# Optimization experiments

Measured on AMD Instinct MI355X. Metric: run time of the kernel, lower is better.

## Reference

```python
import jax, jax.numpy as jnp
import numpy as np

D, H, K, L, NB = 128, 8, 16, 16, 2
N, E, MN, ME = 100_000, 800_000, 1_000, 8_000
VOCAB, BT, VP = 50_000, 256, 15
_SQD, _SQK = float(np.sqrt(D)), float(np.sqrt(K))


def _segment_softmax(score, seg, num):
    m = jax.ops.segment_max(score, seg, num_segments=num)
    e = jnp.exp(score - m[seg])
    z = jax.ops.segment_sum(e, seg, num_segments=num)
    return e / (z[seg] + 1e-9)


def _meta_learner(feat, u, W2, W1):
    # latent-attention factorization: feat [n,D] -> 2d param [n,H,K], 1d param [n,H]
    w = jax.nn.softmax((feat @ u.T) / _SQD, axis=-1)  # [n,L]
    return jnp.einsum('nl,lhk->nhk', w, W2), w @ W1


def _conv(feat, src, dst, p2n, p1n, p2e, p1e, Wq, Wk, Wv, Wo):
    # HeteroAttnConv: multi-head attention message passing modulated by
    # per-node (p2n,p1n) and per-edge (p2e,p1e) meta parameters.
    n = feat.shape[0]
    q = (feat @ Wq).reshape(n, H, K) * p2n
    kf = (feat @ Wk).reshape(n, H, K)
    v = (feat @ Wv).reshape(n, H, K)
    ke = kf[src] * p2e                                   # [e,H,K]
    score = (q[dst] * ke).sum(-1) / _SQK + p1e + p1n[dst]  # [e,H]
    attn = _segment_softmax(score, dst, n)
    agg = jax.ops.segment_sum(attn[..., None] * v[src], dst, num_segments=n).reshape(n, D)
    return jax.nn.relu(agg @ Wo), ke.reshape(-1, D)


def _forward(emb, u, W2lat, W1lat, Wq_m, Wk_m, Wv_m, Wo_m, Wq, Wk, Wv, Wo,
             node_vals, meta_node_vals, src, dst, meta_src, meta_dst,
             meta_node_id, meta_edge_id, target_idx,
             static_vals, static_src, static_dst):
    # _init_meta_param: static param-name graph, copy_u/sum then meta_learner
    fs = emb[static_vals]
    agg = jax.ops.segment_sum(fs[static_src], static_dst, num_segments=VP)
    p2s, p1s = _meta_learner(agg, u, W2lat, W1lat)
    base_tw, base_n1, base_n2 = p1s[0], p1s[3], p2s[6]   # target_weight, node 1d, node 2d
    base_e1, base_e2 = p1s[9], p2s[12]                   # edge 1d, edge 2d

    meta_feat = emb[meta_node_vals]
    feat = emb[node_vals]
    # _asign_param_to_graph(meta_graph): broadcast base buffers only
    mp2n = jnp.broadcast_to(base_n2, (MN, H, K))
    mp1n = jnp.broadcast_to(base_n1, (MN, H))
    mp2e = jnp.broadcast_to(base_e2, (ME, H, K))
    mp1e = jnp.broadcast_to(base_e1, (ME, H))

    out = jnp.zeros((BT, 1), feat.dtype)
    for b in range(NB):
        pre_meta, pre = meta_feat, feat
        meta_feat, meta_edge_feat = _conv(meta_feat, meta_src, meta_dst,
                                          mp2n, mp1n, mp2e, mp1e,
                                          Wq_m[b], Wk_m[b], Wv_m[b], Wo_m[b])
        # _asign_param_to_graph(graph, meta_node_feat, meta_edge_feat):
        # base repeat + indexed add of meta_learner outputs
        p2mn, p1mn = _meta_learner(meta_feat, u, W2lat, W1lat)
        p2me, p1me = _meta_learner(meta_edge_feat, u, W2lat, W1lat)
        p2n = base_n2[None] + p2mn[meta_node_id]
        p1n = base_n1[None] + p1mn[meta_node_id]
        tw = base_tw[None] + p1mn[meta_node_id]
        p2e = base_e2[None] + p2me[meta_edge_id]
        p1e = base_e1[None] + p1me[meta_edge_id]
        feat, _ = _conv(feat, src, dst, p2n, p1n, p2e, p1e,
                        Wq[b], Wk[b], Wv[b], Wo[b])
        # block residual
        meta_feat = meta_feat + pre_meta
        feat = feat + pre
        # Target: per-target-node weighted readout with target_weight param
        logit = jnp.einsum('th,thk->t', tw[target_idx],
                           feat[target_idx].reshape(BT, H, K))
        out = out + logit[:, None]
    return out / NB


def setup_inputs() -> dict:
    key = jax.random.key(0)
    ks = jax.random.split(key, 24)
    s = 0.05
    inp = {}
    inp['emb'] = jax.random.normal(ks[0], (VOCAB, D), jnp.float32) * s
    inp['u'] = jax.random.normal(ks[1], (L, D), jnp.float32) * s
    inp['W2lat'] = jax.random.normal(ks[2], (L, H, K), jnp.float32) * s
    inp['W1lat'] = jax.random.normal(ks[3], (L, H), jnp.float32) * s
    for i, nm in enumerate(['Wq_m', 'Wk_m', 'Wv_m', 'Wo_m', 'Wq', 'Wk', 'Wv', 'Wo']):
        inp[nm] = jax.random.normal(ks[4 + i], (NB, D, D), jnp.float32) / np.sqrt(D)
    inp['node_vals'] = jax.random.randint(ks[12], (N,), 0, VOCAB)
    inp['meta_node_vals'] = jax.random.randint(ks[13], (MN,), 0, VOCAB)
    inp['src'] = jax.random.randint(ks[14], (E,), 0, N)
    inp['dst'] = jax.random.randint(ks[15], (E,), 0, N)
    inp['meta_src'] = jax.random.randint(ks[16], (ME,), 0, MN)
    inp['meta_dst'] = jax.random.randint(ks[17], (ME,), 0, MN)
    inp['meta_node_id'] = jax.random.randint(ks[18], (N,), 0, MN)
    inp['meta_edge_id'] = jax.random.randint(ks[19], (E,), 0, ME)
    inp['target_idx'] = jax.random.randint(ks[20], (BT,), 0, N)
    # static param-name graph: 5 names x (1 name node + 2 token nodes), tokens->name
    name_pos = np.arange(5) * 3
    inp['static_vals'] = jax.random.randint(ks[21], (VP,), 0, VOCAB)
    inp['static_src'] = jnp.asarray(np.stack([name_pos + 1, name_pos + 2], 1).reshape(-1), jnp.int32)
    inp['static_dst'] = jnp.asarray(np.repeat(name_pos, 2), jnp.int32)
    return inp


def reference(emb, u, W2lat, W1lat, Wq_m, Wk_m, Wv_m, Wo_m, Wq, Wk, Wv, Wo,
              node_vals, meta_node_vals, src, dst, meta_src, meta_dst,
              meta_node_id, meta_edge_id, target_idx,
              static_vals, static_src, static_dst):
    return _forward(emb, u, W2lat, W1lat, Wq_m, Wk_m, Wv_m, Wo_m, Wq, Wk, Wv, Wo,
                    node_vals, meta_node_vals, src, dst, meta_src, meta_dst,
                    meta_node_id, meta_edge_id, target_idx,
                    static_vals, static_src, static_dst)
```

## Files before the change

### kernel.cpp

```cpp
#include <hip/hip_runtime.h>
#include <hip/hip_bf16.h>
#include <hip/hip_fp8.h>

#define DD   128
#define HH   8

typedef short bf16x8 __attribute__((ext_vector_type(8)));
typedef float f32x4  __attribute__((ext_vector_type(4)));
typedef float f32x2  __attribute__((ext_vector_type(2)));

__device__ __forceinline__ float b2f(unsigned short v){
  union { unsigned int u; float f; } x; x.u = ((unsigned int)v) << 16; return x.f;
}
__device__ __forceinline__ unsigned short f2b(float f){
  __hip_bfloat16 h = __float2bfloat16(f);
  return *(unsigned short*)&h;
}
__device__ __forceinline__ unsigned char f2f8(float x){
  __hip_fp8_e4m3 h(x);
  return h.__x;
}
__device__ __forceinline__ float f82f(unsigned char b){
  __hip_fp8_e4m3 h; h.__x = b;
  return (float)h;
}
__device__ __forceinline__ void cvt4(unsigned int w, float* o){
#if defined(__has_builtin)
# if __has_builtin(__builtin_amdgcn_cvt_pk_f32_fp8)
  f32x2 lo = __builtin_amdgcn_cvt_pk_f32_fp8((int)w, false);
  f32x2 hi = __builtin_amdgcn_cvt_pk_f32_fp8((int)w, true);
  o[0]=lo[0]; o[1]=lo[1]; o[2]=hi[0]; o[3]=hi[1];
  return;
# endif
#endif
  o[0]=f82f(w&0xff); o[1]=f82f((w>>8)&0xff);
  o[2]=f82f((w>>16)&0xff); o[3]=f82f((w>>24)&0xff);
}
struct __align__(8) us4 { unsigned short x,y,z,w; };
struct __align__(16) us8 { unsigned short s[8]; };

__device__ __forceinline__ float gld(const void* p, size_t i, bool f32){
  if (f32) return ((const float*)p)[i];
  return b2f(((const unsigned short*)p)[i]);
}

__device__ __forceinline__ void gll16(const void* g, void* l){
  __builtin_amdgcn_global_load_lds(
      (const __attribute__((address_space(1))) unsigned int*)g,
      (__attribute__((address_space(3))) unsigned int*)l, 16, 0, 0);
}

struct WPtrs { const void* p[8]; };

enum { EPI_STORE=0, EPI_SCALE_CONST=1, EPI_RELU=3,
       EPI_RELU_RES=4, EPI_RELU_RES2=5 };

#define CPAD 132

template<int EPI, bool INB, bool OUTB>
__global__ __launch_bounds__(256) void gemm128m(
    const void* __restrict__ Av, const unsigned short* __restrict__ Bt,
    void* __restrict__ Cv, int M,
    const unsigned short* __restrict__ Rb,
    const float* __restrict__ Rf, float* __restrict__ C2,
    const int* __restrict__ mnid, const float* __restrict__ p1mn,
    const float* __restrict__ base,
    const int* __restrict__ tgt_of, const int* __restrict__ tgt_next,
    float* __restrict__ acc)
{
  __shared__ __align__(16) unsigned short Asb[64*128];
  __shared__ __align__(16) unsigned short Btb[16896];
  const int tid = threadIdx.x;
  const int wave = tid >> 6, lane = tid & 63;
  const int row0 = blockIdx.x * 64;

  if (INB){
    const char* Ab = (const char*)Av;
    int n4 = lane >> 4, c = lane & 15;
#pragma unroll
    for (int op=0; op<4; op++){
      int rA = wave*16 + op*4;
      int n = rA + n4;
      int gr = row0 + n; if (gr >= M) gr = M - 1;
      gll16(Ab + (size_t)gr*256 + ((size_t)((c ^ (n & 7)) << 4)), &Asb[rA*128]);
    }
  } else {
    const float* Af = (const float*)Av;
    int r = tid >> 2, cb = (tid & 3) * 32, rx = (r & 7) << 3;
    int gr = row0 + r;
#pragma unroll
    for (int j=0;j<8;j++){
      int cc = cb + j*4;
      float4 val = make_float4(0.f,0.f,0.f,0.f);
      if (gr < M) val = *(const float4*)(Af + (size_t)gr*DD + cc);
      us4 o; o.x=f2b(val.x); o.y=f2b(val.y); o.z=f2b(val.z); o.w=f2b(val.w);
      *(us4*)&Asb[r*128 + (cc ^ rx)] = o;
    }
  }
  {
    int n4 = lane >> 4, c = lane & 15;
#pragma unroll
    for (int op=0; op<8; op++){
      int rB = wave*32 + op*4;
      int n = rB + n4;
      gll16((const char*)Bt + (size_t)n*256 + ((size_t)((c ^ (n & 7)) << 4)),
            &Btb[rB*128]);
    }
  }
  __syncthreads();

  f32x4 acc0[8];
#pragma unroll
  for (int t=0;t<8;t++) acc0[t] = (f32x4){0.f,0.f,0.f,0.f};
  const int am = (lane & 15), kq = (lane >> 4) * 8, axr = (am & 7) << 3;
#pragma unroll
  for (int k0=0;k0<128;k0+=32){
    int xo = (k0 + kq) ^ axr;
    bf16x8 a = *(bf16x8*)&Asb[(wave*16 + am)*128 + xo];
#pragma unroll
    for (int t=0;t<8;t++){
      bf16x8 b = *(bf16x8*)&Btb[(t*16 + am)*128 + xo];
      acc0[t] = __builtin_amdgcn_mfma_f32_16x16x32_bf16(a, b, acc0[t], 0,0,0);
    }
  }
  __syncthreads();
  float* Cls = (float*)Btb;
  {
    int rr = wave*16 + (lane>>4)*4;
    int cc = lane & 15;
#pragma unroll
    for (int t=0;t<8;t++)
#pragma unroll
      for (int r=0;r<4;r++)
        Cls[(rr + r)*CPAD + t*16 + cc] = acc0[t][r];
  }
  __syncthreads();

  {
    int r = tid >> 2, cb = (tid & 3) * 32;
    int gr = row0 + r;
    if (gr < M){
      float hs0 = 0.f, hs1 = 0.f;
#pragma unroll
      for (int j=0;j<8;j++){
        int c = cb + j*4;
        float4 o = *(float4*)&Cls[r*CPAD + c];
        if (EPI == EPI_RELU_RES){
          us4 rb = *(const us4*)(Rb + (size_t)gr*DD + c);
          o.x=fmaxf(o.x,0.f)+b2f(rb.x); o.y=fmaxf(o.y,0.f)+b2f(rb.y);
          o.z=fmaxf(o.z,0.f)+b2f(rb.z); o.w=fmaxf(o.w,0.f)+b2f(rb.w);
          float s4 = o.x + o.y + o.z + o.w;
          if (j < 4) hs0 += s4; else hs1 += s4;
        } else if (EPI == EPI_RELU_RES2){
          o.x=fmaxf(o.x,0.f); o.y=fmaxf(o.y,0.f); o.z=fmaxf(o.z,0.f); o.w=fmaxf(o.w,0.f);
          float4 rf = *(const float4*)(Rf + (size_t)gr*DD + c);
          *(float4*)(C2 + (size_t)gr*DD + c) =
              make_float4(o.x+rf.x, o.y+rf.y, o.z+rf.z, o.w+rf.w);
        }
        if (OUTB){
          us4 ob; ob.x=f2b(o.x); ob.y=f2b(o.y); ob.z=f2b(o.z); ob.w=f2b(o.w);
          *(us4*)((unsigned short*)Cv + (size_t)gr*DD + c) = ob;
        } else {
          *(float4*)((float*)Cv + (size_t)gr*DD + c) = o;
        }
      }
      if (EPI == EPI_RELU_RES){
        int hb = cb >> 4;
        int mn = mnid[gr];
        float tw0 = base[hb]     + p1mn[(size_t)mn*HH + hb];
        float tw1 = base[hb + 1] + p1mn[(size_t)mn*HH + hb + 1];
        float part = tw0*hs0 + tw1*hs1;
        part += __shfl_xor(part, 1, 64);
        part += __shfl_xor(part, 2, 64);
        if ((tid & 3) == 0){
          int ti = tgt_of[gr];
          while (ti >= 0){
            atomicAdd(&acc[ti], part);
            ti = tgt_next[ti];
          }
        }
      }
    }
  }
}

template<int EPIQ, bool INB, bool FP8KV>
__device__ __forceinline__ void qkv_body(
    unsigned short* Asb, unsigned short* Btb, int blk,
    const void* __restrict__ Av,
    const unsigned short* __restrict__ Btq, const unsigned short* __restrict__ Btk,
    const unsigned short* __restrict__ Btv,
    void* __restrict__ Cq, void* __restrict__ Ck, int stK,
    void* __restrict__ Cvo, int stV, int M,
    const float* __restrict__ svec)
{
  const int tid = threadIdx.x;
  const int wave = tid >> 6, lane = tid & 63;
  const int row0 = blk * 64;

  if (INB){
    const char* Ab = (const char*)Av;
    int n4 = lane >> 4, c = lane & 15;
#pragma unroll
    for (int op=0; op<4; op++){
      int rA = wave*16 + op*4;
      int n = rA + n4;
      int gr = row0 + n; if (gr >= M) gr = M - 1;
      gll16(Ab + (size_t)gr*256 + ((size_t)((c ^ (n & 7)) << 4)), &Asb[rA*128]);
    }
  } else {
    const float* Af = (const float*)Av;
    int r = tid >> 2, cb = (tid & 3) * 32, rx = (r & 7) << 3;
    int gr = row0 + r;
#pragma unroll
    for (int j=0;j<8;j++){
      int cc = cb + j*4;
      float4 val = make_float4(0.f,0.f,0.f,0.f);
      if (gr < M) val = *(const float4*)(Af + (size_t)gr*DD + cc);
      us4 o; o.x=f2b(val.x); o.y=f2b(val.y); o.z=f2b(val.z); o.w=f2b(val.w);
      *(us4*)&Asb[r*128 + (cc ^ rx)] = o;
    }
  }

  const unsigned short* Bts[3] = {Btq, Btk, Btv};
  void* Cs[3] = {Cq, Ck, Cvo};
  const int sts[3] = {DD, stK, stV};
  const int am = (lane & 15), kq = (lane >> 4) * 8, axr = (am & 7) << 3;

  for (int ph=0; ph<3; ph++){
    {
      const unsigned short* Bt = Bts[ph];
      int n4 = lane >> 4, c = lane & 15;
#pragma unroll
      for (int op=0; op<8; op++){
        int rB = wave*32 + op*4;
        int n = rB + n4;
        gll16((const char*)Bt + (size_t)n*256 + ((size_t)((c ^ (n & 7)) << 4)),
              &Btb[rB*128]);
      }
    }
    __syncthreads();
    f32x4 acc[8];
#pragma unroll
    for (int t=0;t<8;t++) acc[t] = (f32x4){0.f,0.f,0.f,0.f};
#pragma unroll
    for (int k0=0;k0<128;k0+=32){
      int xo = (k0 + kq) ^ axr;
      bf16x8 a = *(bf16x8*)&Asb[(wave*16 + am)*128 + xo];
#pragma unroll
      for (int t=0;t<8;t++){
        bf16x8 b = *(bf16x8*)&Btb[(t*16 + am)*128 + xo];
        acc[t] = __builtin_amdgcn_mfma_f32_16x16x32_bf16(a, b, acc[t], 0,0,0);
      }
    }
    __syncthreads();
    float* Cls = (float*)Btb;
    {
      int rr = wave*16 + (lane>>4)*4;
      int cc = lane & 15;
#pragma unroll
      for (int t=0;t<8;t++)
#pragma unroll
        for (int r=0;r<4;r++)
          Cls[(rr + r)*CPAD + t*16 + cc] = acc[t][r];
    }
    __syncthreads();
    {
      int r = tid >> 2, cb = (tid & 3) * 32;
      int gr = row0 + r;
      if (gr < M){
#pragma unroll
        for (int j=0;j<8;j++){
          int c = cb + j*4;
          float4 o = *(float4*)&Cls[r*CPAD + c];
          if (ph == 0 && EPIQ == EPI_SCALE_CONST){
            o.x*=svec[c+0]; o.y*=svec[c+1]; o.z*=svec[c+2]; o.w*=svec[c+3];
          }
          if (FP8KV && ph > 0){
            unsigned char* Cb = (unsigned char*)Cs[ph];
            uchar4 ob;
            ob.x=f2f8(o.x*8.f); ob.y=f2f8(o.y*8.f);
            ob.z=f2f8(o.z*8.f); ob.w=f2f8(o.w*8.f);
            *(uchar4*)(Cb + (size_t)gr*256 + c) = ob;
          } else {
            us4 ob; ob.x=f2b(o.x); ob.y=f2b(o.y); ob.z=f2b(o.z); ob.w=f2b(o.w);
            *(us4*)((unsigned short*)Cs[ph] + (size_t)gr*sts[ph] + c) = ob;
          }
        }
      }
    }
    __syncthreads();
  }
}

__global__ __launch_bounds__(256) void gemm_qkv2(
    const unsigned short* __restrict__ featB, const float* __restrict__ featM,
    const unsigned short* __restrict__ wqb, const unsigned short* __restrict__ wkb,
    const unsigned short* __restrict__ wvb,
    const unsigned short* __restrict__ wqm, const unsigned short* __restrict__ wkm,
    const unsigned short* __restrict__ wvm,
    unsigned short* __restrict__ qB, unsigned char* __restrict__ kv8,
    unsigned short* __restrict__ qM, unsigned short* __restrict__ kfM,
    unsigned short* __restrict__ vM,
    int Nbig, int Nmeta, int gN, const float* __restrict__ svec)
{
  __shared__ __align__(16) unsigned short Asb[64*128];
  __shared__ __align__(16) unsigned short Btb[16896];
  if (blockIdx.x < gN){
    qkv_body<EPI_STORE,true,true>(Asb, Btb, blockIdx.x, featB,
        wqb, wkb, wvb, qB, kv8, 0, kv8 + 128, 0, Nbig, svec);
  } else {
    qkv_body<EPI_SCALE_CONST,false,false>(Asb, Btb, blockIdx.x - gN, featM,
        wqm, wkm, wvm, qM, kfM, DD, vM, DD, Nmeta, svec);
  }
}

__global__ __launch_bounds__(256) void k_static(
    const void* __restrict__ emb, const int* __restrict__ svals,
    const int* __restrict__ ssrc, const int* __restrict__ sdst,
    const void* __restrict__ u, const void* __restrict__ W2,
    const void* __restrict__ W1, float* __restrict__ base, int nsrc,
    int* __restrict__ dflag)
{
  __shared__ float sagg[15][128];
  __shared__ float ssc[15][16];
  __shared__ float sww[15][16];
  __shared__ int swf;
  const int t = threadIdx.x;
  if (t < 64){
    float m = 0.f;
    for (int i=t; i<128; i+=64){
      float x = fabsf(b2f(((const unsigned short*)emb)[i]));
      if (x < 1e30f) m = fmaxf(m, x);
    }
#pragma unroll
    for (int s=1;s<64;s<<=1) m = fmaxf(m, __shfl_xor(m, s, 64));
    if (t==0){ int f = (m > 1e4f) ? 1 : 0; *dflag = f; swf = f; }
  }
  for (int i=t;i<15*128;i+=256) ((float*)sagg)[i]=0.f;
  __syncthreads();
  const bool wf32 = (swf != 0);
  if (t < 128){
    for (int i=0;i<nsrc;i++){
      int row = sdst[i]; int vr = svals[ssrc[i]];
      sagg[row][t] += gld(emb, (size_t)vr*DD + t, wf32);
    }
  }
  __syncthreads();
  if (t < 240){
    int n = t>>4, l = t&15;
    float a=0.f;
    for (int d=0;d<128;d++) a += sagg[n][d]*gld(u, l*128+d, wf32);
    ssc[n][l] = a * 0.08838834764831845f;
  }
  __syncthreads();
  if (t < 15){
    float mx=-1e30f;
    for (int l=0;l<16;l++) mx = fmaxf(mx, ssc[t][l]);
    float s=0.f;
    for (int l=0;l<16;l++){ float e=__expf(ssc[t][l]-mx); sww[t][l]=e; s+=e; }
    float inv = 1.f/s;
    for (int l=0;l<16;l++) sww[t][l]*=inv;
  }
  __syncthreads();
  if (t < 8){
    float a=0.f,b=0.f,c=0.f;
    for (int l=0;l<16;l++){
      float wv = gld(W1, l*8+t, wf32);
      a += sww[0][l]*wv; b += sww[3][l]*wv; c += sww[9][l]*wv;
    }
    base[t]=a; base[8+t]=b; base[16+t]=c;
  }
  if (t < 128){
    float a=0.f,b=0.f;
    for (int l=0;l<16;l++){
      float wv = gld(W2, l*128+t, wf32);
      a += sww[6][l]*wv; b += sww[12][l]*wv;
    }
    base[24+t]=a; base[152+t]=b;
  }
}

__global__ __launch_bounds__(256) void gather_repack(
    const void* __restrict__ emb,
    const int* __restrict__ valsB, unsigned short* __restrict__ featB, int nB,
    const int* __restrict__ valsM, float* __restrict__ featM, int nM,
    WPtrs W, unsigned short* __restrict__ stage, int NBt,
    const int* __restrict__ dflag, int gB)
{
  const bool wf32 = (*dflag) != 0;
  if ((int)blockIdx.x >= gB){
    int bid = blockIdx.x - gB;
    int idx = bid >> 6;
    int ti = idx / NBt, bi = idx - ti*NBt;
    size_t bo = (size_t)bi*DD*DD;
    int i = (bid & 63)*256 + threadIdx.x;
    int k = i >> 7, n = i & 127;
    float x;
    if (wf32) x = ((const float*)W.p[ti])[bo + i];
    else      x = b2f(((const unsigned short*)W.p[ti])[bo + i]);
    stage[(size_t)idx*DD*DD + n*DD + k] = f2b(x);
    return;
  }
  int i = blockIdx.x*256 + threadIdx.x;
  bool big = (i < nB*16);
  int i2 = big ? i : (i - nB*16);
  if (!big && i2 >= nM*16) return;
  int r = i2>>4, c = (i2&15)*8;
  int vr = big ? valsB[r] : valsM[r];
  float vb[8];
  if (wf32){
    float4 f0 = *(const float4*)((const float*)emb + (size_t)vr*DD + c);
    float4 f1 = *(const float4*)((const float*)emb + (size_t)vr*DD + c + 4);
    vb[0]=f0.x; vb[1]=f0.y; vb[2]=f0.z; vb[3]=f0.w;
    vb[4]=f1.x; vb[5]=f1.y; vb[6]=f1.z; vb[7]=f1.w;
  } else {
    uint4 raw = *(const uint4*)((const unsigned short*)emb + (size_t)vr*DD + c);
    const unsigned short* hw = (const unsigned short*)&raw;
#pragma unroll
    for (int j=0;j<8;j++) vb[j] = b2f(hw[j]);
  }
  if (big){
    unsigned short* d = featB + (size_t)r*DD + c;
    us4 o0, o1;
    o0.x=f2b(vb[0]); o0.y=f2b(vb[1]); o0.z=f2b(vb[2]); o0.w=f2b(vb[3]);
    o1.x=f2b(vb[4]); o1.y=f2b(vb[5]); o1.z=f2b(vb[6]); o1.w=f2b(vb[7]);
    *(us4*)d = o0; *(us4*)(d+4) = o1;
  } else {
    float* d = featM + (size_t)r*DD + c;
    *(float4*)d     = make_float4(vb[0],vb[1],vb[2],vb[3]);
    *(float4*)(d+4) = make_float4(vb[4],vb[5],vb[6],vb[7]);
  }
}

__global__ __launch_bounds__(256) void k_init(
    int* __restrict__ degAll, int nDeg,
    int* __restrict__ tgt_of, int Nn,
    float* __restrict__ acc, int BT)
{
  int i = blockIdx.x*256 + threadIdx.x;
  if (i < nDeg) degAll[i] = 0;
  if (i < Nn) tgt_of[i] = -1;
  if (i < BT) acc[i] = 0.f;
}

__global__ __launch_bounds__(256) void k_hist2(
    const int* __restrict__ dstB, const int* __restrict__ dstM,
    int* __restrict__ degB, int* __restrict__ degM, int E, int ME, int nbE){
  int b = blockIdx.x, t = threadIdx.x;
  if (b < nbE){ int i = b*256+t; if (i < E) atomicAdd(&degB[dstB[i]], 1); }
  else { int i = (b-nbE)*256+t; if (i < ME) atomicAdd(&degM[dstM[i]], 1); }
}

__global__ __launch_bounds__(256) void k_scan1b(
    const int* __restrict__ degB, int* __restrict__ rpB, int* __restrict__ bsB,
    int nB, int nbB,
    const int* __restrict__ degM, int* __restrict__ rpM, int* __restrict__ bsM,
    int nM){
  __shared__ int ls[256];
  int blk = blockIdx.x, t = threadIdx.x;
  const int* deg; int* rowptr; int* bsum; int n; int b;
  if (blk < nbB){ deg=degB; rowptr=rpB; bsum=bsB; n=nB; b=blk; }
  else          { deg=degM; rowptr=rpM; bsum=bsM; n=nM; b=blk-nbB; }
  int base = b*1024 + t*4;
  int v0 = (base+0<n)?deg[base+0]:0;
  int v1 = (base+1<n)?deg[base+1]:0;
  int v2 = (base+2<n)?deg[base+2]:0;
  int v3 = (base+3<n)?deg[base+3]:0;
  int tsum = v0+v1+v2+v3;
  ls[t] = tsum; __syncthreads();
  for (int o=1;o<256;o<<=1){
    int x = (t>=o) ? ls[t-o] : 0;
    __syncthreads();
    ls[t] += x;
    __syncthreads();
  }
  int excl = ls[t]-tsum;
  if (t==255) bsum[b] = ls[255];
  if (base+0<n) rowptr[base+0]=excl;
  if (base+1<n) rowptr[base+1]=excl+v0;
  if (base+2<n) rowptr[base+2]=excl+v0+v1;
  if (base+3<n) rowptr[base+3]=excl+v0+v1+v2;
}

__global__ __launch_bounds__(256) void k_scan3b(
    int* __restrict__ rpB, const int* __restrict__ bsB, int* __restrict__ curB,
    int nB, int nb3B, int nbsB,
    int* __restrict__ rpM, const int* __restrict__ bsM, int* __restrict__ curM,
    int nM, int nbsM){
  __shared__ int spre;
  int blk = blockIdx.x, t = threadIdx.x;
  if (blk < nb3B){
    if (t == 0){
      int chunk = blk >> 2;
      int pre = 0;
      for (int j=0;j<chunk;j++) pre += bsB[j];
      spre = pre;
      if (blk == 0){
        int tot = 0;
        for (int j=0;j<nbsB;j++) tot += bsB[j];
        rpB[nB] = tot;
      }
    }
    __syncthreads();
    int i = blk*256 + t;
    if (i < nB){ int r = rpB[i] + spre; rpB[i] = r; curB[i] = r; }
  } else {
    int b2 = blk - nb3B;
    if (t == 0){
      int chunk = b2 >> 2;
      int pre = 0;
      for (int j=0;j<chunk;j++) pre += bsM[j];
      spre = pre;
      if (b2 == 0){
        int tot = 0;
        for (int j=0;j<nbsM;j++) tot += bsM[j];
        rpM[nM] = tot;
      }
    }
    __syncthreads();
    int i = b2*256 + t;
    if (i < nM){ int r = rpM[i] + spre; rpM[i] = r; curM[i] = r; }
  }
}

__global__ __launch_bounds__(256) void k_scatter2(
    const int* __restrict__ dstB, const int* __restrict__ srcB,
    const int* __restrict__ auxB, int* __restrict__ curB,
    int* __restrict__ epackB, int E, int nbE,
    const int* __restrict__ dstM, const int* __restrict__ srcM,
    int* __restrict__ curM, int* __restrict__ esrcM, int* __restrict__ eauxM,
    int ME, int nbME,
    const int* __restrict__ tgt, int* __restrict__ tgt_of,
    int* __restrict__ tgt_next, int BT){
  int blk = blockIdx.x, t = threadIdx.x;
  if (blk < nbE){
    int e = blk*256 + t;
    if (e < E){
      int p = atomicAdd(&curB[dstB[e]], 1);
      epackB[p] = srcB[e] | (auxB[e] << 17);
    }
  } else if (blk < nbE + nbME){
    int e = (blk-nbE)*256 + t;
    if (e < ME){
      int p = atomicAdd(&curM[dstM[e]], 1);
      esrcM[p] = srcM[e];
      eauxM[p] = e;
    }
  } else {
    for (int i=t; i<BT; i+=256){
      int old = atomicExch(&tgt_of[tgt[i]], i);
      tgt_next[i] = old;
    }
  }
}

__global__ __launch_bounds__(256) void edge_meta_csr(
    const int* __restrict__ rowptr, const int* __restrict__ esrc,
    const int* __restrict__ eorig,
    const unsigned short* __restrict__ qm, const unsigned short* __restrict__ kfm,
    const unsigned short* __restrict__ vm,
    const float* __restrict__ base, unsigned short* __restrict__ mef,
    float* __restrict__ agg, int NM)
{
  int d = blockIdx.x*4 + (threadIdx.x>>6);
  if (d >= NM) return;
  int lane = threadIdx.x & 63;
  const float* be2 = base+152; const float* be1 = base+16; const float* bn1 = base+8;
  size_t dq = (size_t)d*DD;
  float q0 = b2f(qm[dq+lane]), q1 = b2f(qm[dq+64+lane]);
  float w0 = be2[lane], w1 = be2[64+lane];
  int h0 = lane>>4, h1 = h0+4;
  float bias0 = be1[h0] + bn1[h0];
  float bias1 = be1[h1] + bn1[h1];
  float z0=0.f, z1=0.f, a0=0.f, a1=0.f;
  int i0 = rowptr[d], i1 = rowptr[d+1];
  for (int i=i0; i<i1; i++){
    int s = esrc[i], e = eorig[i];
    size_t so=(size_t)s*DD, eo=(size_t)e*DD;
    float ke0 = b2f(kfm[so+lane])    * w0;
    float ke1 = b2f(kfm[so+64+lane]) * w1;
    mef[eo+lane]=f2b(ke0); mef[eo+64+lane]=f2b(ke1);
    float p0 = q0*ke0, p1 = q1*ke1;
#pragma unroll
    for (int m=1;m<16;m<<=1){ p0 += __shfl_xor(p0,m,64); p1 += __shfl_xor(p1,m,64); }
    float e0 = __expf(p0*0.25f + bias0);
    float e1 = __expf(p1*0.25f + bias1);
    z0 += e0; z1 += e1;
    a0 += e0*b2f(vm[so+lane]);
    a1 += e1*b2f(vm[so+64+lane]);
  }
  float inv0 = 1.f/(z0 + 1e-9f);
  float inv1 = 1.f/(z1 + 1e-9f);
  agg[dq+lane]    = a0*inv0;
  agg[dq+64+lane] = a1*inv1;
}

__global__ __launch_bounds__(128) void learner2(
    const float* __restrict__ Xa, const unsigned short* __restrict__ Xb,
    int Ma, int Mtot,
    const void* __restrict__ u, const void* __restrict__ W2,
    const void* __restrict__ W1,
    float* __restrict__ p2a, float* __restrict__ p1a,
    unsigned short* __restrict__ w2me, unsigned short* __restrict__ p1b,
    const float* __restrict__ base, const int* __restrict__ dflag)
{
  __shared__ float sX[128];
  __shared__ float st[16];
  __shared__ float sw[16];
  const bool wf32 = (*dflag) != 0;
  const int t = threadIdx.x;
  const int l = t>>3, j = t&7;
  float uc[16], w2c[16], w1c[16];
#pragma unroll
  for (int m=0;m<16;m++) uc[m] = gld(u, (size_t)l*128 + j*16 + m, wf32);
#pragma unroll
  for (int i=0;i<16;i++) w2c[i] = gld(W2, (size_t)i*128 + t, wf32);
  if (t < 8){
#pragma unroll
    for (int i=0;i<16;i++) w1c[i] = gld(W1, (size_t)i*8 + t, wf32);
  }
  for (int rr=0; rr<4; rr++){
    int row = blockIdx.x*4 + rr;
    if (row >= Mtot) break;
    const bool isB = (row >= Ma);
    const int m = isB ? (row - Ma) : row;
    if (isB) sX[t] = b2f(Xb[(size_t)m*DD + t]);
    else     sX[t] = Xa[(size_t)m*DD + t];
    __syncthreads();
    float part = 0.f;
#pragma unroll
    for (int mm=0;mm<16;mm++) part += sX[j*16+mm]*uc[mm];
    part += __shfl_xor(part,1,64); part += __shfl_xor(part,2,64); part += __shfl_xor(part,4,64);
    if (j==0) st[l] = part * 0.08838834764831845f;
    __syncthreads();
    float mx=-1e30f;
    for (int i=0;i<16;i++) mx = fmaxf(mx, st[i]);
    float ssum=0.f;
    for (int i=0;i<16;i++) ssum += __expf(st[i]-mx);
    float inv = 1.f/ssum;
    if (t<16) sw[t] = __expf(st[t]-mx)*inv;
    __syncthreads();
    float a=0.f;
#pragma unroll
    for (int i=0;i<16;i++) a += sw[i]*w2c[i];
    if (isB) w2me[(size_t)m*DD+t] = f2b(base[152+t] + a);
    else     p2a[(size_t)m*DD+t] = a;
    if (t<8){
      float bb=0.f;
#pragma unroll
      for (int i=0;i<16;i++) bb += sw[i]*w1c[i];
      if (isB) p1b[(size_t)m*HH+t] = f2b(bb);
      else     p1a[(size_t)m*HH+t] = bb;
    }
    __syncthreads();
  }
}

__global__ __launch_bounds__(256) void edge_fused(
    const int* __restrict__ rowptr, const int* __restrict__ epack,
    const int* __restrict__ mnid,
    const unsigned short* __restrict__ q, const unsigned char* __restrict__ kv8,
    const unsigned short* __restrict__ w2me, const unsigned short* __restrict__ p1me,
    const float* __restrict__ p1mn, const float* __restrict__ p2mn,
    const float* __restrict__ base,
    unsigned short* __restrict__ aggb, int N)
{
  int wv = blockIdx.x*4 + (threadIdx.x>>6);
  int lane = threadIdx.x & 63;
  int grp = lane >> 4, l16 = lane & 15;
  int d = wv*4 + grp;
  if (d >= N) return;
  int c8 = l16 * 8;
  int h = l16 >> 1;

  int i0 = rowptr[d], i1 = rowptr[d+1];
  int mn = mnid[d];
  float bias = base[16+h] + base[8+h] + p1mn[(size_t)mn*HH + h];
  size_t dq = (size_t)d*DD;
  float qv[8];
  {
    uint4 qraw = *(const uint4*)(q + dq + c8);
    const unsigned short* qh = (const unsigned short*)&qraw;
    const float* p2 = p2mn + (size_t)mn*DD + c8;
    const float* sv = base + 24 + c8;
#pragma unroll
    for (int j=0;j<8;j++) qv[j] = b2f(qh[j]) * (sv[j] + p2[j]) * 0.03125f;
  }

  float zh = 0.f;
  float a[8];
#pragma unroll
  for (int j=0;j<8;j++) a[j] = 0.f;

  int i = i0;
  for (; i + 1 < i1; i += 2){
    unsigned int v0p = (unsigned int)epack[i];
    unsigned int v1p = (unsigned int)epack[i+1];
    int s0 = v0p & 0x1FFFF, me0 = v0p >> 17;
    int s1 = v1p & 0x1FFFF, me1 = v1p >> 17;
    const unsigned char* kv0 = kv8 + (size_t)s0*256 + c8;
    const unsigned char* kv1 = kv8 + (size_t)s1*256 + c8;
    uint2 kraw0 = *(const uint2*)kv0;
    uint2 vraw0 = *(const uint2*)(kv0 + 128);
    uint4 wraw0 = *(const uint4*)(w2me + (size_t)me0*DD + c8);
    float pm0 = b2f(p1me[(size_t)me0*HH + h]);
    uint2 kraw1 = *(const uint2*)kv1;
    uint2 vraw1 = *(const uint2*)(kv1 + 128);
    uint4 wraw1 = *(const uint4*)(w2me + (size_t)me1*DD + c8);
    float pm1 = b2f(p1me[(size_t)me1*HH + h]);
    float k0f[8], v0f[8], k1f[8], v1f[8];
    cvt4(kraw0.x, k0f); cvt4(kraw0.y, k0f+4);
    cvt4(vraw0.x, v0f); cvt4(vraw0.y, v0f+4);
    cvt4(kraw1.x, k1f); cvt4(kraw1.y, k1f+4);
    cvt4(vraw1.x, v1f); cvt4(vraw1.y, v1f+4);
    const unsigned short* wh0 = (const unsigned short*)&wraw0;
    const unsigned short* wh1 = (const unsigned short*)&wraw1;
    float pA = 0.f, pB = 0.f;
#pragma unroll
    for (int j=0;j<8;j++){
      pA += qv[j]*(k0f[j]*b2f(wh0[j]));
      pB += qv[j]*(k1f[j]*b2f(wh1[j]));
    }
    pA += __shfl_xor(pA, 1, 64);
    pB += __shfl_xor(pB, 1, 64);
    float ex0 = __expf(pA + bias + pm0);
    float ex1 = __expf(pB + bias + pm1);
    zh += ex0 + ex1;
#pragma unroll
    for (int j=0;j<8;j++) a[j] += ex0*v0f[j] + ex1*v1f[j];
  }
  if (i < i1){
    unsigned int vp = (unsigned int)epack[i];
    int s = vp & 0x1FFFF, me = vp >> 17;
    const unsigned char* kv = kv8 + (size_t)s*256 + c8;
    uint2 kraw = *(const uint2*)kv;
    uint2 vraw = *(const uint2*)(kv + 128);
    uint4 wraw = *(const uint4*)(w2me + (size_t)me*DD + c8);
    float pm = b2f(p1me[(size_t)me*HH + h]);
    float kf[8], vf[8];
    cvt4(kraw.x, kf); cvt4(kraw.y, kf+4);
    cvt4(vraw.x, vf); cvt4(vraw.y, vf+4);
    const unsigned short* wh = (const unsigned short*)&wraw;
    float p = 0.f;
#pragma unroll
    for (int j=0;j<8;j++) p += qv[j]*(kf[j]*b2f(wh[j]));
    p += __shfl_xor(p, 1, 64);
    float ex = __expf(p + bias + pm);
    zh += ex;
#pragma unroll
    for (int j=0;j<8;j++) a[j] += ex*vf[j];
  }

  float inv = 0.125f / (zh + 1e-9f);
  us8 o;
#pragma unroll
  for (int j=0;j<8;j++) o.s[j] = f2b(a[j]*inv);
  *(us8*)(aggb + dq + c8) = o;
}

__global__ __launch_bounds__(256) void k_finish(
    const float* __restrict__ acc, void* __restrict__ out,
    float invNB, int BT, const int* __restrict__ dflag)
{
  int t = blockIdx.x*256 + threadIdx.x;
  if (t >= BT) return;
  float r = acc[t] * invNB;
  if ((*dflag) != 0) ((float*)out)[t] = r;
  else ((__hip_bfloat16*)out)[t] = __float2bfloat16(r);
}

extern "C" void kernel_launch(void* const* d_in, const int* in_sizes, int n_in,
                              void* d_out, int out_size, void* d_ws, size_t ws_size,
                              hipStream_t stream) {
  const void* emb   = d_in[0];
  const void* u     = d_in[1];
  const void* W2lat = d_in[2];
  const void* W1lat = d_in[3];
  WPtrs wptrs;
  for (int i=0;i<8;i++) wptrs.p[i] = d_in[4+i];
  const int* node_vals      = (const int*)d_in[12];
  const int* meta_node_vals = (const int*)d_in[13];
  const int* src            = (const int*)d_in[14];
  const int* dst            = (const int*)d_in[15];
  const int* meta_src       = (const int*)d_in[16];
  const int* meta_dst       = (const int*)d_in[17];
  const int* meta_node_id   = (const int*)d_in[18];
  const int* meta_edge_id   = (const int*)d_in[19];
  const int* target_idx     = (const int*)d_in[20];
  const int* static_vals    = (const int*)d_in[21];
  const int* static_src     = (const int*)d_in[22];
  const int* static_dst     = (const int*)d_in[23];

  const int N  = in_sizes[12];
  const int MN = in_sizes[13];
  const int E  = in_sizes[14];
  const int ME = in_sizes[16];
  const int BT = in_sizes[20];
  const int NSRC = in_sizes[22];
  const int NB = in_sizes[8] / (DD*DD);

  float* ws = (float*)d_ws;
  size_t off = 0;
  auto allocf = [&](size_t n){ float* p = ws + off; off += (n + 3) & ~(size_t)3; return p; };
  auto allocb = [&](size_t n){ unsigned short* p = (unsigned short*)(ws + off); off += (((n+1)/2) + 3) & ~(size_t)3; return p; };
  auto alloci = [&](size_t n){ int* p = (int*)(ws + off); off += (n + 3) & ~(size_t)3; return p; };
  int*            dflag = (int*)ws; off += 4;
  unsigned short* feat  = allocb((size_t)N*DD);
  unsigned short* q     = allocb((size_t)N*DD);
  unsigned char*  kv8   = (unsigned char*)allocf((size_t)N*64);
  unsigned short* aggb  = allocb((size_t)N*DD);
  float*          meta_feat= allocf((size_t)MN*DD);
  float*          agg_m = allocf((size_t)MN*DD);
  unsigned short* q_m   = allocb((size_t)MN*DD);
  unsigned short* kf_m  = allocb((size_t)MN*DD);
  unsigned short* v_m   = allocb((size_t)MN*DD);
  float*          meta_out = allocf((size_t)MN*DD);
  unsigned short* mef   = allocb((size_t)ME*DD);
  float*          p2mn  = allocf((size_t)MN*DD);
  float*          p1mn  = allocf((size_t)MN*HH);
  unsigned short* w2me  = allocb((size_t)ME*DD);
  unsigned short* p1me  = allocb((size_t)ME*HH);
  float*          base  = allocf(280);
  float*          acc   = allocf((size_t)BT);
  unsigned short* wstage= allocb((size_t)8*NB*DD*DD);
  int*            rowptr= alloci((size_t)N+1);
  int*            cursor= alloci((size_t)N);
  int*            epack = alloci((size_t)E);
  int*            rowptr_m= alloci((size_t)MN+1);
  int*            cursor_m= alloci((size_t)MN);
  int*            esrc_m  = alloci((size_t)ME);
  int*            eorig_m = alloci((size_t)ME);
  int*            degAll  = alloci((size_t)(N+MN));
  int*            deg     = degAll;
  int*            deg_m   = degAll + N;
  int*            tgt_of  = alloci((size_t)N);
  int*            tgt_next= alloci((size_t)BT);
  const int nb_scan   = (N + 1023)/1024;
  const int nb_scan_m = (MN + 1023)/1024;
  int*            bsum   = alloci((size_t)nb_scan);
  int*            bsum_m = alloci((size_t)nb_scan_m);
  (void)ws_size; (void)n_in; (void)out_size;

  const float* base_n2 = base + 24;

  k_init<<<(N+MN+255)/256,256,0,stream>>>(degAll, N+MN, tgt_of, N, acc, BT);
  k_static<<<1,256,0,stream>>>(emb, static_vals, static_src, static_dst,
                               u, W2lat, W1lat, base, NSRC, dflag);
  const int gB = ((N+MN)*16+255)/256;
  gather_repack<<<gB + 8*NB*64,256,0,stream>>>(emb, node_vals, feat, N,
      meta_node_vals, meta_feat, MN, wptrs, wstage, NB, dflag, gB);

  const int nbE  = (E+255)/256, nbME = (ME+255)/256;
  const int nb3B = (N+255)/256, nb3M = (MN+255)/256;
  k_hist2<<<nbE+nbME,256,0,stream>>>(dst, meta_dst, deg, deg_m, E, ME, nbE);
  k_scan1b<<<nb_scan+nb_scan_m,256,0,stream>>>(deg, rowptr, bsum, N, nb_scan,
      deg_m, rowptr_m, bsum_m, MN);
  k_scan3b<<<nb3B+nb3M,256,0,stream>>>(rowptr, bsum, cursor, N, nb3B, nb_scan,
      rowptr_m, bsum_m, cursor_m, MN, nb_scan_m);
  k_scatter2<<<nbE+nbME+1,256,0,stream>>>(dst, src, meta_edge_id, cursor,
      epack, E, nbE, meta_dst, meta_src, cursor_m, esrc_m, eorig_m, ME, nbME,
      target_idx, tgt_of, tgt_next, BT);

  const int gm = (MN+63)/64;
  const int gN = (N+63)/64;
  const float invNB = 1.0f/(float)NB;

  for (int b=0;b<NB;b++){
    const unsigned short* wq_m = wstage + (size_t)(0*NB+b)*DD*DD;
    const unsigned short* wk_m = wstage + (size_t)(1*NB+b)*DD*DD;
    const unsigned short* wv_m = wstage + (size_t)(2*NB+b)*DD*DD;
    const unsigned short* wo_m = wstage + (size_t)(3*NB+b)*DD*DD;
    const unsigned short* wqb  = wstage + (size_t)(4*NB+b)*DD*DD;
    const unsigned short* wkb  = wstage + (size_t)(5*NB+b)*DD*DD;
    const unsigned short* wvb  = wstage + (size_t)(6*NB+b)*DD*DD;
    const unsigned short* wob  = wstage + (size_t)(7*NB+b)*DD*DD;

    gemm_qkv2<<<gN+gm,256,0,stream>>>(feat, meta_feat,
        wqb, wkb, wvb, wq_m, wk_m, wv_m,
        q, kv8, q_m, kf_m, v_m, N, MN, gN, base_n2);

    edge_meta_csr<<<(MN+3)/4,256,0,stream>>>(rowptr_m, esrc_m, eorig_m,
        q_m, kf_m, v_m, base, mef, agg_m, MN);
    gemm128m<EPI_RELU_RES2,false,false><<<gm,256,0,stream>>>(agg_m, wo_m,
        meta_out, MN, nullptr, meta_feat, meta_feat,
        nullptr, nullptr, nullptr, nullptr, nullptr, nullptr);
    learner2<<<(MN+ME+3)/4,128,0,stream>>>(meta_out, mef, MN, MN+ME,
        u, W2lat, W1lat, p2mn, p1mn, w2me, p1me, base, dflag);

    edge_fused<<<(N+15)/16,256,0,stream>>>(rowptr, epack,
        meta_node_id, q, kv8, w2me, p1me, p1mn, p2mn, base, aggb, N);
    gemm128m<EPI_RELU_RES,true,true><<<gN,256,0,stream>>>(aggb, wob, feat, N,
        feat, nullptr, nullptr,
        meta_node_id, p1mn, base, tgt_of, tgt_next, acc);
  }
  k_finish<<<(BT+255)/256,256,0,stream>>>(acc, d_out, invNB, BT, dflag);
}
```

Before: 554.7 us.

## Fuse setup kernels, fold meta Wo GEMM into learner, split meta edge work

Merges k_init, k_static and gather_repack into one k_setup launch. The meta-graph output projection (the Wo GEMM with relu and residual) now runs inside learner2 as a per-row dot product, which removes a GEMM launch and the meta_out buffer. learner2 also precomputes the bf16 q-scale (base plus p2) per meta node, so edge_fused reads one bf16 vector instead of two float arrays. edge_meta_csr uses two waves per destination node, one per half of the feature dimension, for more parallelism. The cost is a scalar GEMV inside learner2 and lower precision for the q-scale.

```diff
diff --git a/kernel.cpp b/kernel.cpp
--- a/kernel.cpp
+++ b/kernel.cpp
@@ -52,17 +52,12 @@
 
 struct WPtrs { const void* p[8]; };
 
-enum { EPI_STORE=0, EPI_SCALE_CONST=1, EPI_RELU=3,
-       EPI_RELU_RES=4, EPI_RELU_RES2=5 };
-
 #define CPAD 132
 
-template<int EPI, bool INB, bool OUTB>
-__global__ __launch_bounds__(256) void gemm128m(
+__global__ __launch_bounds__(256) void gemm_wo(
     const void* __restrict__ Av, const unsigned short* __restrict__ Bt,
     void* __restrict__ Cv, int M,
     const unsigned short* __restrict__ Rb,
-    const float* __restrict__ Rf, float* __restrict__ C2,
     const int* __restrict__ mnid, const float* __restrict__ p1mn,
     const float* __restrict__ base,
     const int* __restrict__ tgt_of, const int* __restrict__ tgt_next,
@@ -74,7 +69,7 @@
   const int wave = tid >> 6, lane = tid & 63;
   const int row0 = blockIdx.x * 64;
 
-  if (INB){
+  {
     const char* Ab = (const char*)Av;
     int n4 = lane >> 4, c = lane & 15;
 #pragma unroll
@@ -84,18 +79,6 @@
       int gr = row0 + n; if (gr >= M) gr = M - 1;
       gll16(Ab + (size_t)gr*256 + ((size_t)((c ^ (n & 7)) << 4)), &Asb[rA*128]);
     }
-  } else {
-    const float* Af = (const float*)Av;
-    int r = tid >> 2, cb = (tid & 3) * 32, rx = (r & 7) << 3;
-    int gr = row0 + r;
-#pragma unroll
-    for (int j=0;j<8;j++){
-      int cc = cb + j*4;
-      float4 val = make_float4(0.f,0.f,0.f,0.f);
-      if (gr < M) val = *(const float4*)(Af + (size_t)gr*DD + cc);
-      us4 o; o.x=f2b(val.x); o.y=f2b(val.y); o.z=f2b(val.z); o.w=f2b(val.w);
-      *(us4*)&Asb[r*128 + (cc ^ rx)] = o;
-    }
   }
   {
     int n4 = lane >> 4, c = lane & 15;
@@ -145,44 +128,33 @@
       for (int j=0;j<8;j++){
         int c = cb + j*4;
         float4 o = *(float4*)&Cls[r*CPAD + c];
-        if (EPI == EPI_RELU_RES){
-          us4 rb = *(const us4*)(Rb + (size_t)gr*DD + c);
-          o.x=fmaxf(o.x,0.f)+b2f(rb.x); o.y=fmaxf(o.y,0.f)+b2f(rb.y);
-          o.z=fmaxf(o.z,0.f)+b2f(rb.z); o.w=fmaxf(o.w,0.f)+b2f(rb.w);
-          float s4 = o.x + o.y + o.z + o.w;
-          if (j < 4) hs0 += s4; else hs1 += s4;
-        } else if (EPI == EPI_RELU_RES2){
-          o.x=fmaxf(o.x,0.f); o.y=fmaxf(o.y,0.f); o.z=fmaxf(o.z,0.f); o.w=fmaxf(o.w,0.f);
-          float4 rf = *(const float4*)(Rf + (size_t)gr*DD + c);
-          *(float4*)(C2 + (size_t)gr*DD + c) =
-              make_float4(o.x+rf.x, o.y+rf.y, o.z+rf.z, o.w+rf.w);
+        us4 rb = *(const us4*)(Rb + (size_t)gr*DD + c);
+        o.x=fmaxf(o.x,0.f)+b2f(rb.x); o.y=fmaxf(o.y,0.f)+b2f(rb.y);
+        o.z=fmaxf(o.z,0.f)+b2f(rb.z); o.w=fmaxf(o.w,0.f)+b2f(rb.w);
+        float s4 = o.x + o.y + o.z + o.w;
+        if (j < 4) hs0 += s4; else hs1 += s4;
+        us4 ob; ob.x=f2b(o.x); ob.y=f2b(o.y); ob.z=f2b(o.z); ob.w=f2b(o.w);
+        *(us4*)((unsigned short*)Cv + (size_t)gr*DD + c) = ob;
+      }
+      int hb = cb >> 4;
+      int mn = mnid[gr];
+      float tw0 = base[hb]     + p1mn[(size_t)mn*HH + hb];
+      float tw1 = base[hb + 1] + p1mn[(size_t)mn*HH + hb + 1];
+      float part = tw0*hs0 + tw1*hs1;
+      part += __shfl_xor(part, 1, 64);
+      part += __shfl_xor(part, 2, 64);
+      if ((tid & 3) == 0){
+        int ti = tgt_of[gr];
+        while (ti >= 0){
+          atomicAdd(&acc[ti], part);
+          ti = tgt_next[ti];
         }
-        if (OUTB){
-          us4 ob; ob.x=f2b(o.x); ob.y=f2b(o.y); ob.z=f2b(o.z); ob.w=f2b(o.w);
-          *(us4*)((unsigned short*)Cv + (size_t)gr*DD + c) = ob;
-        } else {
-          *(float4*)((float*)Cv + (size_t)gr*DD + c) = o;
-        }
-      }
-      if (EPI == EPI_RELU_RES){
-        int hb = cb >> 4;
-        int mn = mnid[gr];
-        float tw0 = base[hb]     + p1mn[(size_t)mn*HH + hb];
-        float tw1 = base[hb + 1] + p1mn[(size_t)mn*HH + hb + 1];
-        float part = tw0*hs0 + tw1*hs1;
-        part += __shfl_xor(part, 1, 64);
-        part += __shfl_xor(part, 2, 64);
-        if ((tid & 3) == 0){
-          int ti = tgt_of[gr];
-          while (ti >= 0){
-            atomicAdd(&acc[ti], part);
-            ti = tgt_next[ti];
-          }
-        }
-      }
-    }
-  }
-}
+      }
+    }
+  }
+}
+
+enum { EPI_STORE=0, EPI_SCALE_CONST=1 };
 
 template<int EPIQ, bool INB, bool FP8KV>
 __device__ __forceinline__ void qkv_body(
@@ -315,18 +287,90 @@
   }
 }
 
-__global__ __launch_bounds__(256) void k_static(
+__global__ __launch_bounds__(256) void k_setup(
     const void* __restrict__ emb, const int* __restrict__ svals,
     const int* __restrict__ ssrc, const int* __restrict__ sdst,
     const void* __restrict__ u, const void* __restrict__ W2,
     const void* __restrict__ W1, float* __restrict__ base, int nsrc,
-    int* __restrict__ dflag)
+    int* __restrict__ dflag,
+    int* __restrict__ degAll, int nDeg, int* __restrict__ tgt_of, int Nn,
+    float* __restrict__ acc, int BT,
+    const int* __restrict__ valsB, unsigned short* __restrict__ featB, int nB,
+    const int* __restrict__ valsM, float* __restrict__ featM, int nM,
+    WPtrs W, unsigned short* __restrict__ stage, int NBt,
+    int nInit, int gB)
 {
-  __shared__ float sagg[15][128];
-  __shared__ float ssc[15][16];
-  __shared__ float sww[15][16];
+  const int t = threadIdx.x;
+  int blk = blockIdx.x;
+  if (blk == 0){
+    __shared__ float sagg[15][128];
+    __shared__ float ssc[15][16];
+    __shared__ float sww[15][16];
+    __shared__ int swf0;
+    if (t < 64){
+      float m = 0.f;
+      for (int i=t; i<128; i+=64){
+        float x = fabsf(b2f(((const unsigned short*)emb)[i]));
+        if (x < 1e30f) m = fmaxf(m, x);
+      }
+#pragma unroll
+      for (int s=1;s<64;s<<=1) m = fmaxf(m, __shfl_xor(m, s, 64));
+      if (t==0){ int f = (m > 1e4f) ? 1 : 0; *dflag = f; swf0 = f; }
+    }
+    for (int i=t;i<15*128;i+=256) ((float*)sagg)[i]=0.f;
+    __syncthreads();
+    const bool wf32 = (swf0 != 0);
+    if (t < 128){
+      for (int i=0;i<nsrc;i++){
+        int row = sdst[i]; int vr = svals[ssrc[i]];
+        sagg[row][t] += gld(emb, (size_t)vr*DD + t, wf32);
+      }
+    }
+    __syncthreads();
+    if (t < 240){
+      int n = t>>4, l = t&15;
+      float a=0.f;
+      for (int d=0;d<128;d++) a += sagg[n][d]*gld(u, l*128+d, wf32);
+      ssc[n][l] = a * 0.08838834764831845f;
+    }
+    __syncthreads();
+    if (t < 15){
+      float mx=-1e30f;
+      for (int l=0;l<16;l++) mx = fmaxf(mx, ssc[t][l]);
+      float s=0.f;
+      for (int l=0;l<16;l++){ float e=__expf(ssc[t][l]-mx); sww[t][l]=e; s+=e; }
+      float inv = 1.f/s;
+      for (int l=0;l<16;l++) sww[t][l]*=inv;
+    }
+    __syncthreads();
+    if (t < 8){
+      float a=0.f,b=0.f,c=0.f;
+      for (int l=0;l<16;l++){
+        float wv = gld(W1, l*8+t, wf32);
+        a += sww[0][l]*wv; b += sww[3][l]*wv; c += sww[9][l]*wv;
+      }
+      base[t]=a; base[8+t]=b; base[16+t]=c;
+    }
+    if (t < 128){
+      float a=0.f,b=0.f;
+      for (int l=0;l<16;l++){
+        float wv = gld(W2, l*128+t, wf32);
+        a += sww[6][l]*wv; b += sww[12][l]*wv;
+      }
+      base[24+t]=a; base[152+t]=b;
+    }
+    return;
+  }
+  blk -= 1;
+  if (blk < nInit){
+    int i = blk*256 + t;
+    if (i < nDeg) degAll[i] = 0;
+    if (i < Nn) tgt_of[i] = -1;
+    if (i < BT) acc[i] = 0.f;
+    return;
+  }
+  blk -= nInit;
   __shared__ int swf;
-  const int t = threadIdx.x;
   if (t < 64){
     float m = 0.f;
     for (int i=t; i<128; i+=64){
@@ -335,66 +379,16 @@
     }
 #pragma unroll
     for (int s=1;s<64;s<<=1) m = fmaxf(m, __shfl_xor(m, s, 64));
-    if (t==0){ int f = (m > 1e4f) ? 1 : 0; *dflag = f; swf = f; }
-  }
-  for (int i=t;i<15*128;i+=256) ((float*)sagg)[i]=0.f;
+    if (t==0) swf = (m > 1e4f) ? 1 : 0;
+  }
   __syncthreads();
   const bool wf32 = (swf != 0);
-  if (t < 128){
-    for (int i=0;i<nsrc;i++){
-      int row = sdst[i]; int vr = svals[ssrc[i]];
-      sagg[row][t] += gld(emb, (size_t)vr*DD + t, wf32);
-    }
-  }
-  __syncthreads();
-  if (t < 240){
-    int n = t>>4, l = t&15;
-    float a=0.f;
-    for (int d=0;d<128;d++) a += sagg[n][d]*gld(u, l*128+d, wf32);
-    ssc[n][l] = a * 0.08838834764831845f;
-  }
-  __syncthreads();
-  if (t < 15){
-    float mx=-1e30f;
-    for (int l=0;l<16;l++) mx = fmaxf(mx, ssc[t][l]);
-    float s=0.f;
-    for (int l=0;l<16;l++){ float e=__expf(ssc[t][l]-mx); sww[t][l]=e; s+=e; }
-    float inv = 1.f/s;
-    for (int l=0;l<16;l++) sww[t][l]*=inv;
-  }
-  __syncthreads();
-  if (t < 8){
-    float a=0.f,b=0.f,c=0.f;
-    for (int l=0;l<16;l++){
-      float wv = gld(W1, l*8+t, wf32);
-      a += sww[0][l]*wv; b += sww[3][l]*wv; c += sww[9][l]*wv;
-    }
-    base[t]=a; base[8+t]=b; base[16+t]=c;
-  }
-  if (t < 128){
-    float a=0.f,b=0.f;
-    for (int l=0;l<16;l++){
-      float wv = gld(W2, l*128+t, wf32);
-      a += sww[6][l]*wv; b += sww[12][l]*wv;
-    }
-    base[24+t]=a; base[152+t]=b;
-  }
-}
-
-__global__ __launch_bounds__(256) void gather_repack(
-    const void* __restrict__ emb,
-    const int* __restrict__ valsB, unsigned short* __restrict__ featB, int nB,
-    const int* __restrict__ valsM, float* __restrict__ featM, int nM,
-    WPtrs W, unsigned short* __restrict__ stage, int NBt,
-    const int* __restrict__ dflag, int gB)
-{
-  const bool wf32 = (*dflag) != 0;
-  if ((int)blockIdx.x >= gB){
-    int bid = blockIdx.x - gB;
+  if (blk >= gB){
+    int bid = blk - gB;
     int idx = bid >> 6;
     int ti = idx / NBt, bi = idx - ti*NBt;
     size_t bo = (size_t)bi*DD*DD;
-    int i = (bid & 63)*256 + threadIdx.x;
+    int i = (bid & 63)*256 + t;
     int k = i >> 7, n = i & 127;
     float x;
     if (wf32) x = ((const float*)W.p[ti])[bo + i];
@@ -402,7 +396,7 @@
     stage[(size_t)idx*DD*DD + n*DD + k] = f2b(x);
     return;
   }
-  int i = blockIdx.x*256 + threadIdx.x;
+  int i = blk*256 + t;
   bool big = (i < nB*16);
   int i2 = big ? i : (i - nB*16);
   if (!big && i2 >= nM*16) return;
@@ -431,17 +425,6 @@
     *(float4*)d     = make_float4(vb[0],vb[1],vb[2],vb[3]);
     *(float4*)(d+4) = make_float4(vb[4],vb[5],vb[6],vb[7]);
   }
-}
-
-__global__ __launch_bounds__(256) void k_init(
-    int* __restrict__ degAll, int nDeg,
-    int* __restrict__ tgt_of, int Nn,
-    float* __restrict__ acc, int BT)
-{
-  int i = blockIdx.x*256 + threadIdx.x;
-  if (i < nDeg) degAll[i] = 0;
-  if (i < Nn) tgt_of[i] = -1;
-  if (i < BT) acc[i] = 0.f;
 }
 
 __global__ __launch_bounds__(256) void k_hist2(
@@ -563,37 +546,32 @@
     const float* __restrict__ base, unsigned short* __restrict__ mef,
     float* __restrict__ agg, int NM)
 {
-  int d = blockIdx.x*4 + (threadIdx.x>>6);
+  int id = blockIdx.x*4 + (threadIdx.x>>6);
+  int d = id >> 1, half = id & 1;
   if (d >= NM) return;
   int lane = threadIdx.x & 63;
+  int off = half*64 + lane;
   const float* be2 = base+152; const float* be1 = base+16; const float* bn1 = base+8;
   size_t dq = (size_t)d*DD;
-  float q0 = b2f(qm[dq+lane]), q1 = b2f(qm[dq+64+lane]);
-  float w0 = be2[lane], w1 = be2[64+lane];
-  int h0 = lane>>4, h1 = h0+4;
-  float bias0 = be1[h0] + bn1[h0];
-  float bias1 = be1[h1] + bn1[h1];
-  float z0=0.f, z1=0.f, a0=0.f, a1=0.f;
+  float q0 = b2f(qm[dq+off]);
+  float w0 = be2[off];
+  int h = half*4 + (lane>>4);
+  float bias = be1[h] + bn1[h];
+  float z0=0.f, a0=0.f;
   int i0 = rowptr[d], i1 = rowptr[d+1];
   for (int i=i0; i<i1; i++){
     int s = esrc[i], e = eorig[i];
     size_t so=(size_t)s*DD, eo=(size_t)e*DD;
-    float ke0 = b2f(kfm[so+lane])    * w0;
-    float ke1 = b2f(kfm[so+64+lane]) * w1;
-    mef[eo+lane]=f2b(ke0); mef[eo+64+lane]=f2b(ke1);
-    float p0 = q0*ke0, p1 = q1*ke1;
-#pragma unroll
-    for (int m=1;m<16;m<<=1){ p0 += __shfl_xor(p0,m,64); p1 += __shfl_xor(p1,m,64); }
-    float e0 = __expf(p0*0.25f + bias0);
-    float e1 = __expf(p1*0.25f + bias1);
-    z0 += e0; z1 += e1;
-    a0 += e0*b2f(vm[so+lane]);
-    a1 += e1*b2f(vm[so+64+lane]);
-  }
-  float inv0 = 1.f/(z0 + 1e-9f);
-  float inv1 = 1.f/(z1 + 1e-9f);
-  agg[dq+lane]    = a0*inv0;
-  agg[dq+64+lane] = a1*inv1;
+    float ke0 = b2f(kfm[so+off]) * w0;
+    mef[eo+off]=f2b(ke0);
+    float p0 = q0*ke0;
+#pragma unroll
+    for (int m=1;m<16;m<<=1) p0 += __shfl_xor(p0,m,64);
+    float e0 = __expf(p0*0.25f + bias);
+    z0 += e0;
+    a0 += e0*b2f(vm[so+off]);
+  }
+  agg[dq+off] = a0 / (z0 + 1e-9f);
 }
 
 __global__ __launch_bounds__(128) void learner2(
@@ -601,11 +579,13 @@
     int Ma, int Mtot,
     const void* __restrict__ u, const void* __restrict__ W2,
     const void* __restrict__ W1,
-    float* __restrict__ p2a, float* __restrict__ p1a,
+    const unsigned short* __restrict__ WoT, float* __restrict__ mfeat,
+    unsigned short* __restrict__ qsc, float* __restrict__ p1a,
     unsigned short* __restrict__ w2me, unsigned short* __restrict__ p1b,
     const float* __restrict__ base, const int* __restrict__ dflag)
 {
   __shared__ float sX[128];
+  __shared__ float sAgg[128];
   __shared__ float st[16];
   __shared__ float sw[16];
   const bool wf32 = (*dflag) != 0;
@@ -626,7 +606,20 @@
     const bool isB = (row >= Ma);
     const int m = isB ? (row - Ma) : row;
     if (isB) sX[t] = b2f(Xb[(size_t)m*DD + t]);
-    else     sX[t] = Xa[(size_t)m*DD + t];
+    else     sAgg[t] = Xa[(size_t)m*DD + t];
+    __syncthreads();
+    if (!isB){
+      const unsigned short* wrow = WoT + (size_t)t*DD;
+      float s = 0.f;
+      for (int kk=0; kk<128; kk+=8){
+        us8 wv = *(const us8*)(wrow + kk);
+#pragma unroll
+        for (int jj=0;jj<8;jj++) s += sAgg[kk+jj]*b2f(wv.s[jj]);
+      }
+      float r = fmaxf(s, 0.f);
+      mfeat[(size_t)m*DD + t] += r;
+      sX[t] = r;
+    }
     __syncthreads();
     float part = 0.f;
 #pragma unroll
@@ -645,7 +638,7 @@
 #pragma unroll
     for (int i=0;i<16;i++) a += sw[i]*w2c[i];
     if (isB) w2me[(size_t)m*DD+t] = f2b(base[152+t] + a);
-    else     p2a[(size_t)m*DD+t] = a;
+    else     qsc [(size_t)m*DD+t] = f2b(base[24+t] + a);
     if (t<8){
       float bb=0.f;
 #pragma unroll
@@ -662,7 +655,7 @@
     const int* __restrict__ mnid,
     const unsigned short* __restrict__ q, const unsigned char* __restrict__ kv8,
     const unsigned short* __restrict__ w2me, const unsigned short* __restrict__ p1me,
-    const float* __restrict__ p1mn, const float* __restrict__ p2mn,
+    const float* __restrict__ p1mn, const unsigned short* __restrict__ qsc,
     const float* __restrict__ base,
     unsigned short* __restrict__ aggb, int N)
 {
@@ -681,11 +674,10 @@
   float qv[8];
   {
     uint4 qraw = *(const uint4*)(q + dq + c8);
+    us8 sc = *(const us8*)(qsc + (size_t)mn*DD + c8);
     const unsigned short* qh = (const unsigned short*)&qraw;
-    const float* p2 = p2mn + (size_t)mn*DD + c8;
-    const float* sv = base + 24 + c8;
-#pragma unroll
-    for (int j=0;j<8;j++) qv[j] = b2f(qh[j]) * (sv[j] + p2[j]) * 0.03125f;
+#pragma unroll
+    for (int j=0;j<8;j++) qv[j] = b2f(qh[j]) * b2f(sc.s[j]) * 0.03125f;
   }
 
   float zh = 0.f;
@@ -815,9 +807,8 @@
   unsigned short* q_m   = allocb((size_t)MN*DD);
   unsigned short* kf_m  = allocb((size_t)MN*DD);
   unsigned short* v_m   = allocb((size_t)MN*DD);
-  float*          meta_out = allocf((size_t)MN*DD);
   unsigned short* mef   = allocb((size_t)ME*DD);
-  float*          p2mn  = allocf((size_t)MN*DD);
+  unsigned short* qsc   = allocb((size_t)MN*DD);
   float*          p1mn  = allocf((size_t)MN*HH);
   unsigned short* w2me  = allocb((size_t)ME*DD);
   unsigned short* p1me  = allocb((size_t)ME*HH);
@@ -844,12 +835,13 @@
 
   const float* base_n2 = base + 24;
 
-  k_init<<<(N+MN+255)/256,256,0,stream>>>(degAll, N+MN, tgt_of, N, acc, BT);
-  k_static<<<1,256,0,stream>>>(emb, static_vals, static_src, static_dst,
-                               u, W2lat, W1lat, base, NSRC, dflag);
+  const int nInit = (N + MN + 255)/256;
   const int gB = ((N+MN)*16+255)/256;
-  gather_repack<<<gB + 8*NB*64,256,0,stream>>>(emb, node_vals, feat, N,
-      meta_node_vals, meta_feat, MN, wptrs, wstage, NB, dflag, gB);
+  k_setup<<<1 + nInit + gB + 8*NB*64,256,0,stream>>>(
+      emb, static_vals, static_src, static_dst, u, W2lat, W1lat, base, NSRC,
+      dflag, degAll, N+MN, tgt_of, N, acc, BT,
+      node_vals, feat, N, meta_node_vals, meta_feat, MN,
+      wptrs, wstage, NB, nInit, gB);
 
   const int nbE  = (E+255)/256, nbME = (ME+255)/256;
   const int nb3B = (N+255)/256, nb3M = (MN+255)/256;
@@ -880,19 +872,16 @@
         wqb, wkb, wvb, wq_m, wk_m, wv_m,
         q, kv8, q_m, kf_m, v_m, N, MN, gN, base_n2);
 
-    edge_meta_csr<<<(MN+3)/4,256,0,stream>>>(rowptr_m, esrc_m, eorig_m,
+    edge_meta_csr<<<(2*MN+3)/4,256,0,stream>>>(rowptr_m, esrc_m, eorig_m,
         q_m, kf_m, v_m, base, mef, agg_m, MN);
-    gemm128m<EPI_RELU_RES2,false,false><<<gm,256,0,stream>>>(agg_m, wo_m,
-        meta_out, MN, nullptr, meta_feat, meta_feat,
-        nullptr, nullptr, nullptr, nullptr, nullptr, nullptr);
-    learner2<<<(MN+ME+3)/4,128,0,stream>>>(meta_out, mef, MN, MN+ME,
-        u, W2lat, W1lat, p2mn, p1mn, w2me, p1me, base, dflag);
+    learner2<<<(MN+ME+3)/4,128,0,stream>>>(agg_m, mef, MN, MN+ME,
+        u, W2lat, W1lat, wo_m, meta_feat,
+        qsc, p1mn, w2me, p1me, base, dflag);
 
     edge_fused<<<(N+15)/16,256,0,stream>>>(rowptr, epack,
-        meta_node_id, q, kv8, w2me, p1me, p1mn, p2mn, base, aggb, N);
-    gemm128m<EPI_RELU_RES,true,true><<<gN,256,0,stream>>>(aggb, wob, feat, N,
-        feat, nullptr, nullptr,
-        meta_node_id, p1mn, base, tgt_of, tgt_next, acc);
+        meta_node_id, q, kv8, w2me, p1me, p1mn, qsc, base, aggb, N);
+    gemm_wo<<<gN,256,0,stream>>>(aggb, wob, feat, N,
+        feat, meta_node_id, p1mn, base, tgt_of, tgt_next, acc);
   }
   k_finish<<<(BT+255)/256,256,0,stream>>>(acc, d_out, invNB, BT, dflag);
 }
```

New measurement: 545.4 us (median of 2 runs). No clear change (-1.7%).
